# Kernel optimization log

Hardware: AMD Instinct MI355X
Metric: run time of the kernel (lower is better)

The kernel has to match this reference:

```python
import jax, jax.numpy as jnp
import numpy as np

def _round_ste(x):
    # StraightThrough: forward = round, backward = identity
    return x + jax.lax.stop_gradient(jnp.round(x) - x)

def setup_inputs() -> dict:
    key = jax.random.key(0)
    k1, k2, k3, k4, k5 = jax.random.split(key, 5)
    in_f, out_f, n_tok = 4096, 4096, 8192
    return {
        "input": jax.random.normal(k1, (n_tok, in_f), dtype=jnp.float32),
        "weight": jax.random.normal(k2, (out_f, in_f), dtype=jnp.float32),
        "bias": jax.random.normal(k3, (out_f,), dtype=jnp.float32),
        "w_scale": jax.random.uniform(k4, (1,), dtype=jnp.float32),
        "b_scale": jax.random.uniform(k5, (1,), dtype=jnp.float32),
    }

def reference(input, weight, bias, w_scale, b_scale):
    # straight-through rounding of quantized latents (use_straight_through=True, compress_bias=True)
    w_q = _round_ste(weight)
    b_q = _round_ste(bias)
    # decoder: per-tensor affine dequantization
    w_dec = w_scale * w_q          # [out, in]
    b_dec = b_scale * b_q          # [out]
    # F.linear: input @ weight.T + bias
    return jnp.einsum('ni,oi->no', input, w_dec) + b_dec
```

## Files before the change

### kernel.cpp

```cpp
#include <hip/hip_runtime.h>
#include <stdint.h>


using bf16x8   = __attribute__((ext_vector_type(8))) __bf16;
using floatx16 = __attribute__((ext_vector_type(16))) float;
using us8      = __attribute__((ext_vector_type(8))) unsigned short;
using us4      = __attribute__((ext_vector_type(4))) unsigned short;

__device__ __forceinline__ unsigned short f2bf_rne(float x) {
    unsigned int u = __float_as_uint(x);
    return (unsigned short)((u + 0x7fffu + ((u >> 16) & 1u)) >> 16);
}

__device__ __forceinline__ void stage16(const unsigned short* g, unsigned short* l) {
    __builtin_amdgcn_global_load_lds(
        (__attribute__((address_space(1))) void*)g,
        (__attribute__((address_space(3))) void*)l,
        16, 0, 0);
}

__global__ __launch_bounds__(256) void cvt_both(
    const float* __restrict__ inA, unsigned short* __restrict__ outA, long long nA4,
    const float* __restrict__ inB, unsigned short* __restrict__ outB, long long nB4) {
    const long long i = (long long)blockIdx.x * 256 + threadIdx.x;
    if (i < nA4) {
        float4 v = ((const float4*)inA)[i];
        us4 o = { f2bf_rne(v.x), f2bf_rne(v.y), f2bf_rne(v.z), f2bf_rne(v.w) };
        ((us4*)outA)[i] = o;
    } else {
        const long long j = i - nA4;
        if (j < nB4) {
            float4 v = ((const float4*)inB)[j];
            us4 o = { f2bf_rne(rintf(v.x)), f2bf_rne(rintf(v.y)),
                      f2bf_rne(rintf(v.z)), f2bf_rne(rintf(v.w)) };
            ((us4*)outB)[j] = o;
        }
    }
}

__global__ __launch_bounds__(512) void gemm256_8ph(
    const unsigned short* __restrict__ A,
    const unsigned short* __restrict__ B,
    const float* __restrict__ bias,
    const float* __restrict__ wscale_p,
    const float* __restrict__ bscale_p,
    float* __restrict__ C,
    int M, int N, int K) {
    constexpr int BK   = 64;
    constexpr int TILE = 256 * BK;
    __shared__ unsigned short ldsA[2 * TILE];
    __shared__ unsigned short ldsB[2 * TILE];

    const int tid  = threadIdx.x;
    const int wave = tid >> 6;
    const int lane = tid & 63;

    const int nbx = N >> 8;
    int wg;
    {
        const int cpx = (int)gridDim.x >> 3;
        wg = ((int)blockIdx.x & 7) * cpx + ((int)blockIdx.x >> 3);
    }
    const int bm = (wg / nbx) << 8;
    const int bn = (wg % nbx) << 8;

    const int wm    = (wave >> 2) << 7;
    const int wn    = (wave & 3) << 6;
    const int col   = lane & 31;
    const int khalf = lane >> 5;

    const int row512 = tid >> 3;
    const int gk = ((tid & 7) ^ (row512 & 7)) << 3;
    const unsigned short* gA = A + (size_t)(bm + row512) * K + gk;
    const unsigned short* gB = B + (size_t)(bn + row512) * K + gk;
    unsigned short* sA = ldsA + (wave << 9);
    unsigned short* sB = ldsB + (wave << 9);

    int rowA[4], rowB[2], slotv[4];
#pragma unroll
    for (int mi = 0; mi < 4; ++mi) rowA[mi] = (wm + mi * 32 + col) << 6;
#pragma unroll
    for (int ni = 0; ni < 2; ++ni) rowB[ni] = (wn + ni * 32 + col) << 6;
#pragma unroll
    for (int ks = 0; ks < 4; ++ks) slotv[ks] = ((ks * 2 + khalf) ^ (col & 7)) << 3;

    const float wsc = wscale_p[0];
    const float bsc = bscale_p[0];
    float badd[2];
#pragma unroll
    for (int ni = 0; ni < 2; ++ni)
        badd[ni] = bsc * rintf(bias[bn + wn + ni * 32 + col]);

    const int NT = K >> 6;

#pragma unroll
    for (int i = 0; i < 4; ++i) {
        stage16(gA + (size_t)(i * 64) * K,      sA + i * 4096);
        stage16(gB + (size_t)(i * 64) * K,      sB + i * 4096);
    }
#pragma unroll
    for (int i = 0; i < 4; ++i) {
        stage16(gA + (size_t)(i * 64) * K + 64, sA + TILE + i * 4096);
        stage16(gB + (size_t)(i * 64) * K + 64, sB + TILE + i * 4096);
    }
    asm volatile("s_waitcnt vmcnt(8)" ::: "memory");
    __builtin_amdgcn_s_barrier();
    __builtin_amdgcn_sched_barrier(0);

    floatx16 acc[4][2] = {};

#define READ_KS(ks, ar, br)                                                       \
    {                                                                             \
        const int so = slotv[ks];                                                 \
        _Pragma("unroll") for (int mi = 0; mi < 4; ++mi)                          \
            ar[mi] = __builtin_bit_cast(bf16x8, *(const us8*)&SA[rowA[mi] + so]); \
        _Pragma("unroll") for (int ni = 0; ni < 2; ++ni)                          \
            br[ni] = __builtin_bit_cast(bf16x8, *(const us8*)&SB[rowB[ni] + so]); \
    }

#define MFMA8(ar, br)                                                             \
    __builtin_amdgcn_s_setprio(1);                                                \
    _Pragma("unroll") for (int mi = 0; mi < 4; ++mi)                              \
        _Pragma("unroll") for (int ni = 0; ni < 2; ++ni)                          \
            acc[mi][ni] = __builtin_amdgcn_mfma_f32_32x32x16_bf16(                \
                ar[mi], br[ni], acc[mi][ni], 0, 0, 0);                            \
    __builtin_amdgcn_s_setprio(0);

    for (int t = 0; t < NT; ++t) {
        const unsigned short* SA = ldsA + (t & 1) * TILE;
        const unsigned short* SB = ldsB + (t & 1) * TILE;
        unsigned short* dA = sA + (t & 1) * TILE;
        unsigned short* dB = sB + (t & 1) * TILE;
        const size_t kt2 = (size_t)(t + 2) * BK;
        const bool do_stage = (t + 2 < NT);

        bf16x8 a0[4], a1[4], a2[4], a3[4];
        bf16x8 b0[2], b1[2], b2[2], b3[2];

        READ_KS(0, a0, b0)
        READ_KS(1, a1, b1)
        MFMA8(a0, b0)
        __builtin_amdgcn_sched_barrier(0);

        READ_KS(2, a2, b2)
        READ_KS(3, a3, b3)
        MFMA8(a1, b1)

        asm volatile("s_waitcnt lgkmcnt(0)" ::: "memory");
        __builtin_amdgcn_sched_barrier(0);
        __builtin_amdgcn_s_barrier();
        __builtin_amdgcn_sched_barrier(0);

        if (do_stage) {
#pragma unroll
            for (int i = 0; i < 2; ++i) {
                stage16(gA + (size_t)(i * 64) * K + kt2, dA + i * 4096);
                stage16(gB + (size_t)(i * 64) * K + kt2, dB + i * 4096);
            }
        }
        MFMA8(a2, b2)
        __builtin_amdgcn_sched_barrier(0);

        if (do_stage) {
#pragma unroll
            for (int i = 2; i < 4; ++i) {
                stage16(gA + (size_t)(i * 64) * K + kt2, dA + i * 4096);
                stage16(gB + (size_t)(i * 64) * K + kt2, dB + i * 4096);
            }
        }
        MFMA8(a3, b3)
        __builtin_amdgcn_sched_barrier(0);

        if (do_stage)         { asm volatile("s_waitcnt vmcnt(8)" ::: "memory"); }
        else if (t + 2 == NT) { asm volatile("s_waitcnt vmcnt(0)" ::: "memory"); }
        __builtin_amdgcn_s_barrier();
        __builtin_amdgcn_sched_barrier(0);
    }

#undef READ_KS
#undef MFMA8

    const int rb = khalf << 2;
#pragma unroll
    for (int mi = 0; mi < 4; ++mi) {
#pragma unroll
        for (int ni = 0; ni < 2; ++ni) {
            const int n = bn + wn + ni * 32 + col;
#pragma unroll
            for (int reg = 0; reg < 16; ++reg) {
                const int m = bm + wm + mi * 32 + (reg & 3) + 8 * (reg >> 2) + rb;
                C[(size_t)m * N + n] = acc[mi][ni][reg] * wsc + badd[ni];
            }
        }
    }
}

__global__ __launch_bounds__(256) void gemm_bf16_bt(
    const unsigned short* __restrict__ A,
    const unsigned short* __restrict__ B,
    const float* __restrict__ bias,
    const float* __restrict__ wscale_p,
    const float* __restrict__ bscale_p,
    float* __restrict__ C,
    int M, int N, int K) {
    constexpr int BM = 128, BK = 64;
    __shared__ unsigned short ldsA[BM * BK];
    __shared__ unsigned short ldsB[BM * BK];

    const int tid  = threadIdx.x;
    const int wave = tid >> 6;
    const int lane = tid & 63;

    const int bm = blockIdx.y * BM;
    const int bn = blockIdx.x * BM;
    const int wm = (wave >> 1) * 64;
    const int wn = (wave & 1) * 64;

    const float wsc = wscale_p[0];
    const float bsc = bscale_p[0];

    const int col = lane & 31;
    const int khalf = lane >> 5;

    float badd[2];
#pragma unroll
    for (int ni = 0; ni < 2; ++ni)
        badd[ni] = bsc * rintf(bias[bn + wn + ni * 32 + col]);

    const int g_st = ((lane & 7) ^ (lane >> 3)) * 8;
    const unsigned short* gAp[4];
    const unsigned short* gBp[4];
    unsigned short* lA[4];
    unsigned short* lB[4];
#pragma unroll
    for (int i = 0; i < 4; ++i) {
        const int r = wave * 32 + i * 8 + (lane >> 3);
        gAp[i] = A + (size_t)(bm + r) * K + g_st;
        gBp[i] = B + (size_t)(bn + r) * K + g_st;
        lA[i] = &ldsA[(wave * 256 + i * 64) * 8];
        lB[i] = &ldsB[(wave * 256 + i * 64) * 8];
    }

    floatx16 acc[2][2] = {};

    for (int kt = 0; kt < K; kt += BK) {
#pragma unroll
        for (int i = 0; i < 4; ++i) {
            stage16(gAp[i] + kt, lA[i]);
            stage16(gBp[i] + kt, lB[i]);
        }
        __syncthreads();

#pragma unroll
        for (int ks = 0; ks < 4; ++ks) {
            const int gc = ks * 2 + khalf;
            const int slot = (gc ^ (lane & 7)) * 8;
            bf16x8 af[2], bfr[2];
#pragma unroll
            for (int mi = 0; mi < 2; ++mi) {
                const int off = (wm + mi * 32 + col) * BK + slot;
                af[mi] = __builtin_bit_cast(bf16x8, *(const us8*)&ldsA[off]);
            }
#pragma unroll
            for (int ni = 0; ni < 2; ++ni) {
                const int off = (wn + ni * 32 + col) * BK + slot;
                bfr[ni] = __builtin_bit_cast(bf16x8, *(const us8*)&ldsB[off]);
            }
#pragma unroll
            for (int mi = 0; mi < 2; ++mi)
#pragma unroll
                for (int ni = 0; ni < 2; ++ni)
                    acc[mi][ni] = __builtin_amdgcn_mfma_f32_32x32x16_bf16(
                        af[mi], bfr[ni], acc[mi][ni], 0, 0, 0);
        }
        __syncthreads();
    }

    const int rbase = 4 * khalf;
#pragma unroll
    for (int mi = 0; mi < 2; ++mi) {
#pragma unroll
        for (int ni = 0; ni < 2; ++ni) {
            const int n = bn + wn + ni * 32 + col;
#pragma unroll
            for (int reg = 0; reg < 16; ++reg) {
                const int m = bm + wm + mi * 32 + (reg & 3) + 8 * (reg >> 2) + rbase;
                C[(size_t)m * N + n] = acc[mi][ni][reg] * wsc + badd[ni];
            }
        }
    }
}

__global__ __launch_bounds__(256) void fallback_gemm(
    const float* __restrict__ A, const float* __restrict__ W,
    const float* __restrict__ bias, const float* __restrict__ wsp,
    const float* __restrict__ bsp, float* __restrict__ C, int M, int N, int K) {
    const int n = blockIdx.x * 256 + threadIdx.x;
    const int m = blockIdx.y;
    if (n >= N || m >= M) return;
    float s = 0.f;
    for (int k = 0; k < K; ++k)
        s += A[(size_t)m * K + k] * rintf(W[(size_t)n * K + k]);
    C[(size_t)m * N + n] = s * wsp[0] + bsp[0] * rintf(bias[n]);
}

extern "C" void kernel_launch(void* const* d_in, const int* in_sizes, int n_in,
                              void* d_out, int out_size, void* d_ws, size_t ws_size,
                              hipStream_t stream) {
    const float* input  = (const float*)d_in[0];
    const float* weight = (const float*)d_in[1];
    const float* bias   = (const float*)d_in[2];
    const float* wscale = (const float*)d_in[3];
    const float* bscale = (const float*)d_in[4];
    float* out = (float*)d_out;

    const int N = in_sizes[2];
    const int K = in_sizes[1] / N;
    const int M = in_sizes[0] / K;

    const size_t needA = (size_t)M * K * sizeof(unsigned short);
    const size_t needB = (size_t)N * K * sizeof(unsigned short);

    if (ws_size >= needA + needB && (M % 128) == 0 && (N % 128) == 0 &&
        (K % 64) == 0) {
        unsigned short* Abf = (unsigned short*)d_ws;
        unsigned short* Bbf = (unsigned short*)((char*)d_ws + needA);
        const long long nA4 = (long long)M * K / 4;
        const long long nB4 = (long long)N * K / 4;
        const long long nthr = nA4 + nB4;
        cvt_both<<<(unsigned)((nthr + 255) / 256), 256, 0, stream>>>(
            input, Abf, nA4, weight, Bbf, nB4);

        const int nwg256 = (M / 256) * (N / 256);
        if ((M % 256) == 0 && (N % 256) == 0 && (K / 64) >= 4 &&
            (nwg256 % 8) == 0) {
            gemm256_8ph<<<dim3(nwg256), 512, 0, stream>>>(
                Abf, Bbf, bias, wscale, bscale, out, M, N, K);
        } else {
            dim3 grid(N / 128, M / 128);
            gemm_bf16_bt<<<grid, 256, 0, stream>>>(Abf, Bbf, bias, wscale,
                                                   bscale, out, M, N, K);
        }
    } else {
        dim3 grid((N + 255) / 256, M);
        fallback_gemm<<<grid, 256, 0, stream>>>(input, weight, bias, wscale, bscale, out, M, N, K);
    }
}
```

Before: 553.4 us.

## Restructure GEMM main loop into four barrier-separated phases with one-ahead prefetch

Replaces the two-tile-ahead prefetch schedule with a one-tile-ahead scheme. Each K-tile is split into four phases: a small set of LDS fragment reads, barrier, then eight MFMAs. Global-to-LDS loads are interleaved across the phases, so quadrants of the next tile are staged as soon as the current buffer's readers are done. This cuts live fragment registers (Af/Bf instead of four sets of a/b) and spreads memory traffic across the loop. The cost is more barriers per tile and less prefetch distance to hide global latency.

```diff
diff --git a/kernel.cpp b/kernel.cpp
--- a/kernel.cpp
+++ b/kernel.cpp
@@ -38,7 +38,7 @@
     }
 }
 
-__global__ __launch_bounds__(512) void gemm256_8ph(
+__global__ __launch_bounds__(512) void gemm256_ph(
     const unsigned short* __restrict__ A,
     const unsigned short* __restrict__ B,
     const float* __restrict__ bias,
@@ -93,92 +93,115 @@
 
     const int NT = K >> 6;
 
-#pragma unroll
-    for (int i = 0; i < 4; ++i) {
-        stage16(gA + (size_t)(i * 64) * K,      sA + i * 4096);
-        stage16(gB + (size_t)(i * 64) * K,      sB + i * 4096);
-    }
-#pragma unroll
-    for (int i = 0; i < 4; ++i) {
-        stage16(gA + (size_t)(i * 64) * K + 64, sA + TILE + i * 4096);
-        stage16(gB + (size_t)(i * 64) * K + 64, sB + TILE + i * 4096);
-    }
-    asm volatile("s_waitcnt vmcnt(8)" ::: "memory");
+    stage16(gA,                     sA);
+    stage16(gA + (size_t)128 * K,   sA + 2 * 4096);
+    stage16(gB,                     sB);
+    stage16(gB + (size_t)64 * K,    sB + 1 * 4096);
+    stage16(gB + (size_t)128 * K,   sB + 2 * 4096);
+    stage16(gB + (size_t)192 * K,   sB + 3 * 4096);
+    stage16(gA + (size_t)64 * K,    sA + 1 * 4096);
+    stage16(gA + (size_t)192 * K,   sA + 3 * 4096);
+    asm volatile("s_waitcnt vmcnt(2)" ::: "memory");
     __builtin_amdgcn_s_barrier();
     __builtin_amdgcn_sched_barrier(0);
 
     floatx16 acc[4][2] = {};
 
-#define READ_KS(ks, ar, br)                                                       \
-    {                                                                             \
-        const int so = slotv[ks];                                                 \
-        _Pragma("unroll") for (int mi = 0; mi < 4; ++mi)                          \
-            ar[mi] = __builtin_bit_cast(bf16x8, *(const us8*)&SA[rowA[mi] + so]); \
-        _Pragma("unroll") for (int ni = 0; ni < 2; ++ni)                          \
-            br[ni] = __builtin_bit_cast(bf16x8, *(const us8*)&SB[rowB[ni] + so]); \
-    }
-
-#define MFMA8(ar, br)                                                             \
-    __builtin_amdgcn_s_setprio(1);                                                \
-    _Pragma("unroll") for (int mi = 0; mi < 4; ++mi)                              \
-        _Pragma("unroll") for (int ni = 0; ni < 2; ++ni)                          \
-            acc[mi][ni] = __builtin_amdgcn_mfma_f32_32x32x16_bf16(                \
-                ar[mi], br[ni], acc[mi][ni], 0, 0, 0);                            \
-    __builtin_amdgcn_s_setprio(0);
+#define LDA_F(mi, ks) __builtin_bit_cast(bf16x8, *(const us8*)&SA[rowA[mi] + slotv[ks]])
+#define LDB_F(ni, ks) __builtin_bit_cast(bf16x8, *(const us8*)&SB[rowB[ni] + slotv[ks]])
+
+#define PH_BAR_LGKM()                                        \
+    __builtin_amdgcn_s_barrier();                            \
+    asm volatile("s_waitcnt lgkmcnt(0)" ::: "memory");       \
+    __builtin_amdgcn_sched_barrier(0);
+
+#define PH_MFMA(MIB, KSB)                                                     \
+    __builtin_amdgcn_s_setprio(1);                                            \
+    _Pragma("unroll") for (int k2 = 0; k2 < 2; ++k2)                          \
+        _Pragma("unroll") for (int m2 = 0; m2 < 2; ++m2)                      \
+            _Pragma("unroll") for (int ni = 0; ni < 2; ++ni)                  \
+                acc[(MIB) + m2][ni] = __builtin_amdgcn_mfma_f32_32x32x16_bf16(\
+                    Af[m2][k2], Bf[ni][(KSB) + k2], acc[(MIB) + m2][ni],      \
+                    0, 0, 0);                                                 \
+    __builtin_amdgcn_s_setprio(0);                                            \
+    __builtin_amdgcn_sched_barrier(0);
 
     for (int t = 0; t < NT; ++t) {
         const unsigned short* SA = ldsA + (t & 1) * TILE;
         const unsigned short* SB = ldsB + (t & 1) * TILE;
-        unsigned short* dA = sA + (t & 1) * TILE;
-        unsigned short* dB = sB + (t & 1) * TILE;
-        const size_t kt2 = (size_t)(t + 2) * BK;
-        const bool do_stage = (t + 2 < NT);
-
-        bf16x8 a0[4], a1[4], a2[4], a3[4];
-        bf16x8 b0[2], b1[2], b2[2], b3[2];
-
-        READ_KS(0, a0, b0)
-        READ_KS(1, a1, b1)
-        MFMA8(a0, b0)
-        __builtin_amdgcn_sched_barrier(0);
-
-        READ_KS(2, a2, b2)
-        READ_KS(3, a3, b3)
-        MFMA8(a1, b1)
-
-        asm volatile("s_waitcnt lgkmcnt(0)" ::: "memory");
-        __builtin_amdgcn_sched_barrier(0);
+        unsigned short* dA = sA + ((t + 1) & 1) * TILE;
+        unsigned short* dB = sB + ((t + 1) & 1) * TILE;
+        const size_t kt1 = (size_t)(t + 1) * BK;
+        const bool st = (t + 1 < NT);
+
+        bf16x8 Af[2][2];
+        bf16x8 Bf[2][4];
+
+#pragma unroll
+        for (int m2 = 0; m2 < 2; ++m2)
+#pragma unroll
+            for (int k2 = 0; k2 < 2; ++k2) Af[m2][k2] = LDA_F(m2, k2);
+#pragma unroll
+        for (int ni = 0; ni < 2; ++ni)
+#pragma unroll
+            for (int k2 = 0; k2 < 2; ++k2) Bf[ni][k2] = LDB_F(ni, k2);
+        if (st) {
+            stage16(gA + kt1,                   dA);
+            stage16(gA + (size_t)128 * K + kt1, dA + 2 * 4096);
+            stage16(gB + kt1,                   dB);
+            stage16(gB + (size_t)64 * K + kt1,  dB + 1 * 4096);
+        }
+        PH_BAR_LGKM()
+        PH_MFMA(0, 0)
         __builtin_amdgcn_s_barrier();
         __builtin_amdgcn_sched_barrier(0);
 
-        if (do_stage) {
-#pragma unroll
-            for (int i = 0; i < 2; ++i) {
-                stage16(gA + (size_t)(i * 64) * K + kt2, dA + i * 4096);
-                stage16(gB + (size_t)(i * 64) * K + kt2, dB + i * 4096);
-            }
-        }
-        MFMA8(a2, b2)
-        __builtin_amdgcn_sched_barrier(0);
-
-        if (do_stage) {
-#pragma unroll
-            for (int i = 2; i < 4; ++i) {
-                stage16(gA + (size_t)(i * 64) * K + kt2, dA + i * 4096);
-                stage16(gB + (size_t)(i * 64) * K + kt2, dB + i * 4096);
-            }
-        }
-        MFMA8(a3, b3)
-        __builtin_amdgcn_sched_barrier(0);
-
-        if (do_stage)         { asm volatile("s_waitcnt vmcnt(8)" ::: "memory"); }
-        else if (t + 2 == NT) { asm volatile("s_waitcnt vmcnt(0)" ::: "memory"); }
+#pragma unroll
+        for (int m2 = 0; m2 < 2; ++m2)
+#pragma unroll
+            for (int k2 = 0; k2 < 2; ++k2) Af[m2][k2] = LDA_F(m2, 2 + k2);
+#pragma unroll
+        for (int ni = 0; ni < 2; ++ni)
+#pragma unroll
+            for (int k2 = 0; k2 < 2; ++k2) Bf[ni][2 + k2] = LDB_F(ni, 2 + k2);
+        if (st) {
+            stage16(gB + (size_t)128 * K + kt1, dB + 2 * 4096);
+            stage16(gB + (size_t)192 * K + kt1, dB + 3 * 4096);
+        }
+        PH_BAR_LGKM()
+        PH_MFMA(0, 2)
+        asm volatile("s_waitcnt vmcnt(6)" ::: "memory");
         __builtin_amdgcn_s_barrier();
         __builtin_amdgcn_sched_barrier(0);
-    }
-
-#undef READ_KS
-#undef MFMA8
+
+#pragma unroll
+        for (int m2 = 0; m2 < 2; ++m2)
+#pragma unroll
+            for (int k2 = 0; k2 < 2; ++k2) Af[m2][k2] = LDA_F(2 + m2, k2);
+        PH_BAR_LGKM()
+        PH_MFMA(2, 0)
+        __builtin_amdgcn_s_barrier();
+        __builtin_amdgcn_sched_barrier(0);
+
+#pragma unroll
+        for (int m2 = 0; m2 < 2; ++m2)
+#pragma unroll
+            for (int k2 = 0; k2 < 2; ++k2) Af[m2][k2] = LDA_F(2 + m2, 2 + k2);
+        if (st) {
+            stage16(gA + (size_t)64 * K + kt1,  dA + 1 * 4096);
+            stage16(gA + (size_t)192 * K + kt1, dA + 3 * 4096);
+        }
+        PH_BAR_LGKM()
+        PH_MFMA(2, 2)
+        asm volatile("s_waitcnt vmcnt(2)" ::: "memory");
+        __builtin_amdgcn_s_barrier();
+        __builtin_amdgcn_sched_barrier(0);
+    }
+
+#undef LDA_F
+#undef LDB_F
+#undef PH_BAR_LGKM
+#undef PH_MFMA
 
     const int rb = khalf << 2;
 #pragma unroll
@@ -334,7 +357,7 @@
         const int nwg256 = (M / 256) * (N / 256);
         if ((M % 256) == 0 && (N % 256) == 0 && (K / 64) >= 4 &&
             (nwg256 % 8) == 0) {
-            gemm256_8ph<<<dim3(nwg256), 512, 0, stream>>>(
+            gemm256_ph<<<dim3(nwg256), 512, 0, stream>>>(
                 Abf, Bbf, bias, wscale, bscale, out, M, N, K);
         } else {
             dim3 grid(N / 128, M / 128);
```

Measured after the change: 551.0 us. About the same (-0.4%).
